# Optimization experiments

Hardware: AMD Instinct MI355X
Metric: run time of the kernel (lower is better)

The kernel has to match this reference:

```python
import jax, jax.numpy as jnp
import numpy as np
from jax import lax

STRIDES = (8, 16, 32)
NUM_CLASSES = 80
TOPK = 1000
CONF_THRESH = 0.05
NMS_THRESH = 0.6


def setup_inputs() -> dict:
    key = jax.random.key(0)
    ks = jax.random.split(key, 10)
    hw = [(256, 256), (128, 128), (64, 64)]
    inp = {}
    for lv, (h, w) in enumerate(hw):
        inp[f"cls_pred_{lv}"] = jax.random.normal(ks[3 * lv + 0], (NUM_CLASSES, h, w), jnp.float32)
        inp[f"reg_pred_{lv}"] = jax.random.normal(ks[3 * lv + 1], (4, h, w), jnp.float32)
        inp[f"ctn_pred_{lv}"] = jax.random.normal(ks[3 * lv + 2], (1, h, w), jnp.float32)
    inp["scales"] = jax.random.uniform(ks[9], (3,), jnp.float32)
    return inp


def _level_decode(cls_p, reg_p, ctn_p, scale, stride):
    # cls_p: [C,H,W] -> flatten to [M,C] matching torch permute(1,2,0).view(-1,C)
    C, H, W = cls_p.shape
    cls = jnp.transpose(cls_p, (1, 2, 0)).reshape(-1, C)          # [M,C]
    reg = jnp.transpose(reg_p, (1, 2, 0)).reshape(-1, 4)          # [M,4]
    reg = jax.nn.relu(reg * scale) * stride                       # Scale + relu + stride
    ctn = jnp.transpose(ctn_p, (1, 2, 0)).reshape(-1, 1)          # [M,1]
    joint = jnp.sqrt(jax.nn.sigmooid(cls) * jax.nn.sigmoid(ctn)) if False else \
        jnp.sqrt(jax.nn.sigmoid(cls) * jax.nn.sigmoid(ctn))      # [M,C]
    scores = jnp.max(joint, axis=-1)                              # [M]
    labels = jnp.argmax(joint, axis=-1)                           # [M]
    ay, ax = jnp.meshgrid(jnp.arange(H), jnp.arange(W), indexing='ij')
    anchors = (jnp.stack([ax, ay], -1).reshape(-1, 2).astype(cls.dtype) + 0.5) * stride  # [M,2]
    # per-level topk (M > TOPK for all levels here)
    scores, idx = lax.top_k(scores, TOPK)
    labels = labels[idx]
    reg = reg[idx]
    anchors = anchors[idx]
    boxes = jnp.concatenate([anchors - reg[:, :2], anchors + reg[:, 2:]], axis=-1)  # x1y1x2y2
    return scores, labels, boxes


def _nms(boxes, scores):
    # Faithful port of the pure-python NMS: fixed-shape keep mask, sorted order.
    N = boxes.shape[0]
    order = jnp.argsort(-scores)
    b = boxes[order]
    x1, y1, x2, y2 = b[:, 0], b[:, 1], b[:, 2], b[:, 3]
    areas = (x2 - x1) * (y2 - y1)
    xx1 = jnp.maximum(x1[:, None], x1[None, :])
    yy1 = jnp.maximum(y1[:, None], y1[None, :])
    xx2 = jnp.minimum(x2[:, None], x2[None, :])
    yy2 = jnp.minimum(y2[:, None], y2[None, :])
    w = jnp.maximum(1e-10, xx2 - xx1)
    h = jnp.maximum(1e-10, yy2 - yy1)
    inter = w * h
    iou = inter / (areas[:, None] + areas[None, :] - inter + 1e-14)  # [N,N]
    idxs = jnp.arange(N)

    def body(i, keep):
        sup = (iou[i] > NMS_THRESH) & (idxs > i) & keep[i]
        return keep & ~sup

    keep = lax.fori_loop(0, N, body, jnp.ones((N,), bool))
    return order, keep


def reference(cls_pred_0, cls_pred_1, cls_pred_2,
              reg_pred_0, reg_pred_1, reg_pred_2,
              ctn_pred_0, ctn_pred_1, ctn_pred_2, scales):
    cls_l = [cls_pred_0, cls_pred_1, cls_pred_2]
    reg_l = [reg_pred_0, reg_pred_1, reg_pred_2]
    ctn_l = [ctn_pred_0, ctn_pred_1, ctn_pred_2]
    all_s, all_l, all_b = [], [], []
    for lv in range(3):
        s, lb, bx = _level_decode(cls_l[lv], reg_l[lv], ctn_l[lv], scales[lv], float(STRIDES[lv]))
        all_s.append(s); all_l.append(lb); all_b.append(bx)
    scores = jnp.concatenate(all_s)   # [3000]
    labels = jnp.concatenate(all_l)
    boxes = jnp.concatenate(all_b)    # [3000,4]
    order, keep = _nms(boxes, scores)
    scores_s = scores[order]
    labels_s = labels[order]
    boxes_s = boxes[order]
    keep = keep & (scores_s > CONF_THRESH)
    return boxes_s, scores_s, labels_s, keep
```

## Files before the change

kernel.cpp:

```cpp
#include <hip/hip_runtime.h>
#include <cmath>
#include <stdint.h>

#define NPTS   86016
#define NCB    1024
#define K_TOP  1000
#define NOUT   3000
#define NWORDS 47
#define NTILE  47
#define ECAP   8192
#define FCAP   1024
#define SPPB   64
#define SELCAP 4096

#define CH_OFF     0
#define CNT_OFF    (NCB * 3 * 4)
#define MEMSET_BYTES (CNT_OFF + 64)
#define KEYS_OFF   (CNT_OFF + 64)
#define LAB_OFF    (KEYS_OFF + NPTS * 8)
#define STAGE_OFF  (LAB_OFF + NPTS * 4)
#define SURV_OFF   (STAGE_OFF + 3 * 65536 * 8)
#define EDGE_OFF   (SURV_OFF + NOUT * 8 + 64)
#define FLAG_OFF   (EDGE_OFF + ECAP * 4)

__device__ __forceinline__ float sig_f32_stepwise(float x) {
    float e = (float)exp(-(double)x);
    return 1.0f / (1.0f + e);
}

__device__ __forceinline__ void locate(int g, int& lv, int& p, int& HW) {
    if (g < 65536)      { lv = 0; p = g;         HW = 65536; }
    else if (g < 81920) { lv = 1; p = g - 65536; HW = 16384; }
    else                { lv = 2; p = g - 81920; HW = 4096;  }
}

__global__ __launch_bounds__(256) void score_kernel(
        const float* __restrict__ cls0, const float* __restrict__ cls1,
        const float* __restrict__ cls2,
        const float* __restrict__ ctn0, const float* __restrict__ ctn1,
        const float* __restrict__ ctn2,
        unsigned long long* __restrict__ keys, int* __restrict__ labels,
        int* __restrict__ chist,
        int* __restrict__ cnt, unsigned* __restrict__ flags) {
    __shared__ float pm[5 * SPPB], pv[5 * SPPB];
    __shared__ int pidx[5 * SPPB];
    __shared__ int lch[NCB];
    const int tid = threadIdx.x;
    const int base = blockIdx.x * SPPB;
    for (int i = tid; i < NCB; i += 256) lch[i] = 0;
    for (int it = tid; it < 5 * SPPB; it += 256) {
        int c = it / SPPB, pt = it - c * SPPB;
        int g = base + pt, lv, p, HW;
        locate(g, lv, p, HW);
        const float* cls = (lv == 0) ? cls0 : ((lv == 1) ? cls1 : cls2);
        const float* bp = cls + (size_t)c * 16 * HW + p;
        float x[16];
#pragma unroll
        for (int cc = 0; cc < 16; cc++) x[cc] = bp[(size_t)cc * HW];
        float m = -INFINITY, v = -INFINITY; int idx = 0;
#pragma unroll
        for (int cc = 0; cc < 16; cc++)
            if (x[cc] > m) { v = m; m = x[cc]; idx = c * 16 + cc; }
        pm[it] = m; pv[it] = v; pidx[it] = idx;
    }
    __syncthreads();
    if (tid < SPPB) {
        int g = base + tid, lv, p, HW;
        locate(g, lv, p, HW);
        const float* ctn = (lv == 0) ? ctn0 : ((lv == 1) ? ctn1 : ctn2);
        float m = -INFINITY, v = -INFINITY; int idx = 0;
#pragma unroll
        for (int k = 0; k < 5; k++) {
            float bm = pm[k * SPPB + tid];
            float bv = pv[k * SPPB + tid];
            int bidx = pidx[k * SPPB + tid];
            if (bm > m) { v = fmaxf(m, bv); m = bm; idx = bidx; }
        }
        float sc = sig_f32_stepwise(ctn[p]);
        float sM = sig_f32_stepwise(m);
        float jm = __fsqrt_rn(sM * sc);
        float sV = sig_f32_stepwise(v);
        float jv = __fsqrt_rn(sV * sc);
        if (jv == jm) {
            int f = atomicAdd(&cnt[13], 1);
            if (f < FCAP) flags[f] = (unsigned)g;
        }
        unsigned int bits = __float_as_uint(jm);
        keys[g] = ((unsigned long long)bits << 32) | (0xFFFFFFFFu - (unsigned)g);
        labels[g] = idx;
        atomicAdd(&lch[(int)(bits >> 20)], 1);
    }
    __syncthreads();
    int lv0, p0, HW0; locate(base, lv0, p0, HW0);
    for (int i = tid; i < NCB; i += 256) {
        int v = lch[i];
        if (v) atomicAdd(&chist[lv0 * NCB + i], v);
    }
}

__global__ __launch_bounds__(1024) void tcs_kernel(
        const float* __restrict__ cls0, const float* __restrict__ cls1,
        const float* __restrict__ cls2,
        const float* __restrict__ ctn0, const float* __restrict__ ctn1,
        const float* __restrict__ ctn2,
        const unsigned long long* __restrict__ keys,
        const int* __restrict__ chist,
        const unsigned* __restrict__ flags, const int* __restrict__ cnt,
        int* __restrict__ labels,
        unsigned long long* __restrict__ stage,
        unsigned long long* __restrict__ surv) {
    int bid = blockIdx.x, tid = threadIdx.x;
    if (bid == 3) {
        int nf = cnt[13]; if (nf > FCAP) nf = FCAP;
        int wave = tid >> 6, lane = tid & 63;
        for (int f = wave; f < nf; f += 16) {
            int g = (int)flags[f], lv, p, HW;
            locate(g, lv, p, HW);
            const float* cls = (lv == 0) ? cls0 : ((lv == 1) ? cls1 : cls2);
            const float* ctn = (lv == 0) ? ctn0 : ((lv == 1) ? ctn1 : ctn2);
            float sc = sig_f32_stepwise(ctn[p]);
            float bestv = -1.0f; int besti = 127;
            {
                float s = sig_f32_stepwise(cls[(size_t)lane * HW + p]);
                float sj = __fsqrt_rn(s * sc);
                bestv = sj; besti = lane;
            }
            if (lane < 16) {
                int c2 = lane + 64;
                float s = sig_f32_stepwise(cls[(size_t)c2 * HW + p]);
                float sj = __fsqrt_rn(s * sc);
                if (sj > bestv) { bestv = sj; besti = c2; }
            }
            for (int off = 32; off; off >>= 1) {
                float ov = __shfl_xor(bestv, off, 64);
                int   oi = __shfl_xor(besti, off, 64);
                if (ov > bestv || (ov == bestv && oi < besti)) { bestv = ov; besti = oi; }
            }
            if (lane == 0) labels[g] = besti;
        }
        return;
    }
    const int lv = bid;
    const int base = (lv == 0) ? 0 : ((lv == 1) ? 65536 : 81920);
    const int HW = (lv == 0) ? 65536 : ((lv == 1) ? 16384 : 4096);
    unsigned long long* stg = stage + (size_t)lv * 65536;

    __shared__ int part[1024];
    __shared__ int fine[257];
    __shared__ int s_chunk, s_above, sBf, sR;
    __shared__ int sSure, sStage, sCand;
    __shared__ unsigned long long sel[SELCAP];

    if (tid == 0) { sSure = 0; sStage = 0; sCand = 0; }
    part[tid] = chist[lv * NCB + tid];
    __syncthreads();
    for (int off = 1; off < 1024; off <<= 1) {
        int v = part[tid] + ((tid + off < 1024) ? part[tid + off] : 0);
        __syncthreads(); part[tid] = v; __syncthreads();
    }
    int nxt = (tid < 1023) ? part[tid + 1] : 0;
    if (part[tid] >= K_TOP && nxt < K_TOP) { s_chunk = tid; s_above = nxt; }
    if (tid < 257) fine[tid] = 0;
    __syncthreads();
    const int chunk = s_chunk, above = s_above;
    for (int i = tid; i < HW; i += 1024) {
        unsigned long long key = keys[base + i];
        int cb = (int)(key >> 52);
        if (cb > chunk) {
            int k = atomicAdd(&sSure, 1);
            sel[k] = key;
        } else if (cb == chunk) {
            int k = atomicAdd(&sStage, 1);
            stg[k] = key;
            atomicAdd(&fine[(int)(key >> 44) & 255], 1);
        }
    }
    __syncthreads();
    for (int off = 1; off < 256; off <<= 1) {
        int v = 0;
        if (tid < 256) v = fine[tid] + ((tid + off < 256) ? fine[tid + off] : 0);
        __syncthreads(); if (tid < 256) fine[tid] = v; __syncthreads();
    }
    if (tid < 256) {
        int ge    = above + fine[tid];
        int genxt = above + ((tid < 255) ? fine[tid + 1] : 0);
        if (ge >= K_TOP && genxt < K_TOP) {
            sBf = tid;
            sR  = K_TOP - genxt;
        }
    }
    __syncthreads();
    const int Bf = sBf;
    const int nstage = sStage;
    {
        int Ca = above + ((Bf < 255) ? fine[Bf + 1] : 0);
        for (int i = tid; i < nstage; i += 1024) {
            unsigned long long key = stg[i];
            int fb = (int)(key >> 44) & 255;
            if (fb > Bf) {
                int k = atomicAdd(&sSure, 1);
                sel[k] = key;
            } else if (fb == Bf) {
                int k = atomicAdd(&sCand, 1);
                int idx = Ca + k;
                if (idx < SELCAP) sel[idx] = key;
            }
        }
    }
    __syncthreads();
    int tot = sSure + sCand; if (tot > SELCAP) tot = SELCAP;
    int m = 1024; while (m < tot) m <<= 1;
    for (int t = tot + tid; t < m; t += 1024) sel[t] = 0ULL;
    __syncthreads();
    for (int k = 2; k <= m; k <<= 1)
        for (int j = k >> 1; j > 0; j >>= 1) {
            for (int t = tid; t < m; t += 1024) {
                int l = t ^ j;
                if (l > t) {
                    unsigned long long a = sel[t], b = sel[l];
                    if (((t & k) == 0) ? (a < b) : (a > b)) { sel[t] = b; sel[l] = a; }
                }
            }
            __syncthreads();
        }
    if (tid < K_TOP) surv[lv * K_TOP + tid] = sel[tid];
}

__global__ __launch_bounds__(1024) void merge_emit_kernel(
        const unsigned long long* __restrict__ surv,
        const int* __restrict__ labels,
        const float* __restrict__ reg0, const float* __restrict__ reg1,
        const float* __restrict__ reg2,
        const float* __restrict__ scales,
        float* __restrict__ out) {
    __shared__ unsigned long long L[3][1024];
    __shared__ unsigned long long s[NOUT];
    int tid = threadIdx.x;
#pragma unroll
    for (int lv = 0; lv < 3; lv++)
        L[lv][tid] = (tid < K_TOP) ? surv[lv * K_TOP + tid] : 0ULL;
    __syncthreads();
    for (int e = tid; e < NOUT; e += 1024) {
        int a = e / K_TOP, i = e - a * K_TOP;
        unsigned long long key = L[a][i];
        int rank = i;
#pragma unroll
        for (int b = 0; b < 3; b++) {
            if (b == a) continue;
            int lo = 0, hi = K_TOP;
            while (lo < hi) {
                int mid = (lo + hi) >> 1;
                if (L[b][mid] > key) lo = mid + 1; else hi = mid;
            }
            rank += lo;
        }
        s[rank] = key;
    }
    __syncthreads();
    for (int r = tid; r < NOUT; r += 1024) {
        unsigned long long key = s[r];
        unsigned int bits = (unsigned)(key >> 32);
        float score = __uint_as_float(bits);
        unsigned int g = 0xFFFFFFFFu - (unsigned)(key & 0xFFFFFFFFULL);
        int lv, p;
        if (g < 65536u)      { lv = 0; p = (int)g; }
        else if (g < 81920u) { lv = 1; p = (int)g - 65536; }
        else                 { lv = 2; p = (int)g - 81920; }
        const float* rp = (lv == 0) ? reg0 : ((lv == 1) ? reg1 : reg2);
        int HW = (lv == 0) ? 65536 : ((lv == 1) ? 16384 : 4096);
        int W = 256 >> lv;
        float strideF = (float)(8 << lv);
        float scale = scales[lv];
        int x = p & (W - 1);
        int y = p >> (8 - lv);
        float r0 = fmaxf(0.0f, rp[0 * HW + p] * scale) * strideF;
        float r1 = fmaxf(0.0f, rp[1 * HW + p] * scale) * strideF;
        float r2 = fmaxf(0.0f, rp[2 * HW + p] * scale) * strideF;
        float r3 = fmaxf(0.0f, rp[3 * HW + p] * scale) * strideF;
        float ax = ((float)x + 0.5f) * strideF;
        float ay = ((float)y + 0.5f) * strideF;
        out[r * 4 + 0] = ax - r0;
        out[r * 4 + 1] = ay - r1;
        out[r * 4 + 2] = ax + r2;
        out[r * 4 + 3] = ay + r3;
        out[12000 + r] = score;
        out[15000 + r] = (float)labels[g];
    }
}

__global__ __launch_bounds__(256) void edge_kernel(const float* __restrict__ out,
                                                   unsigned* __restrict__ edges_g,
                                                   int* __restrict__ cnt) {
    __shared__ float x1[128], y1[128], x2[128], y2[128];
    int t = blockIdx.x, tid = threadIdx.x;
    int ta = 0, rem = t;
    while (rem >= NTILE - ta) { rem -= NTILE - ta; ta++; }
    int tb = ta + rem;
    if (tid < 64) {
        int gi = ta * 64 + tid;
        if (gi < NOUT) {
            float4 b = ((const float4*)out)[gi];
            x1[tid] = b.x; y1[tid] = b.y; x2[tid] = b.z; y2[tid] = b.w;
        }
    } else if (tid < 128) {
        int gj = tb * 64 + (tid - 64);
        if (gj < NOUT) {
            float4 b = ((const float4*)out)[gj];
            x1[tid] = b.x; y1[tid] = b.y; x2[tid] = b.z; y2[tid] = b.w;
        }
    }
    __syncthreads();
#pragma unroll
    for (int q = 0; q < 16; q++) {
        int idx = q * 256 + tid;
        int ii = idx >> 6, jj = idx & 63;
        int i = ta * 64 + ii, j = tb * 64 + jj;
        if (i < j && j < NOUT) {
            float ai = (x2[ii] - x1[ii]) * (y2[ii] - y1[ii]);
            float aj = (x2[64 + jj] - x1[64 + jj]) * (y2[64 + jj] - y1[64 + jj]);
            float xx1 = fmaxf(x1[ii], x1[64 + jj]), yy1 = fmaxf(y1[ii], y1[64 + jj]);
            float xx2 = fminf(x2[ii], x2[64 + jj]), yy2 = fminf(y2[ii], y2[64 + jj]);
            float ww = fmaxf(1e-10f, xx2 - xx1);
            float hh = fmaxf(1e-10f, yy2 - yy1);
            float inter = ww * hh;
            float iou = inter / (((ai + aj) - inter) + 1e-14f);
            if ((double)iou > 0.6) {
                int e = atomicAdd(&cnt[12], 1);
                if (e < ECAP) edges_g[e] = ((unsigned)i << 12) | (unsigned)j;
            }
        }
    }
}

__global__ __launch_bounds__(1024) void nms_sparse_kernel(
        const unsigned* __restrict__ edges_g,
        const int* __restrict__ cnt,
        const float* __restrict__ scores_s,
        float* __restrict__ keep_out) {
    __shared__ unsigned ed[ECAP];
    __shared__ unsigned long long supLds[NWORDS];
    int tid = threadIdx.x;
    int E = cnt[12]; if (E > ECAP) E = ECAP;
    int m = 1; while (m < E) m <<= 1;
    for (int t = tid; t < m; t += 1024) ed[t] = (t < E) ? edges_g[t] : 0xFFFFFFFFu;
    __syncthreads();
    for (int k = 2; k <= m; k <<= 1)
        for (int j = k >> 1; j > 0; j >>= 1) {
            for (int t = tid; t < m; t += 1024) {
                int l = t ^ j;
                if (l > t) {
                    unsigned a = ed[t], b = ed[l];
                    if (((t & k) == 0) ? (a > b) : (a < b)) { ed[t] = b; ed[l] = a; }
                }
            }
            __syncthreads();
        }
    if (tid < 64) {
        int lane = tid;
        unsigned long long supW = 0ULL;
        int ep = 0;
        for (int c = 0; c < NWORDS; c++) {
            unsigned long long cw = __shfl(supW, c, 64);
            int hi = (c + 1) * 64;
            while (ep < E) {
                unsigned k = ed[ep];
                int i = (int)(k >> 12);
                if (i >= hi) break;
                int j = (int)(k & 4095);
                if (!((cw >> (i & 63)) & 1ULL)) {
                    if ((j >> 6) == c) cw |= 1ULL << (j & 63);
                    else if (lane == (j >> 6)) supW |= 1ULL << (j & 63);
                }
                ep++;
            }
            if (lane == c) supW = cw;
        }
        if (lane < NWORDS) supLds[lane] = supW;
    }
    __syncthreads();
    for (int j = tid; j < NOUT; j += 1024) {
        bool s = (supLds[j >> 6] >> (j & 63)) & 1ULL;
        float scv = scores_s[j];
        keep_out[j] = (!s && ((double)scv > 0.05)) ? 1.0f : 0.0f;
    }
}

extern "C" void kernel_launch(void* const* d_in, const int* in_sizes, int n_in,
                              void* d_out, int out_size, void* d_ws, size_t ws_size,
                              hipStream_t stream) {
    const float* cls0 = (const float*)d_in[0];
    const float* reg0 = (const float*)d_in[1];
    const float* ctn0 = (const float*)d_in[2];
    const float* cls1 = (const float*)d_in[3];
    const float* reg1 = (const float*)d_in[4];
    const float* ctn1 = (const float*)d_in[5];
    const float* cls2 = (const float*)d_in[6];
    const float* reg2 = (const float*)d_in[7];
    const float* ctn2 = (const float*)d_in[8];
    const float* scales = (const float*)d_in[9];

    char* ws = (char*)d_ws;
    int* chist = (int*)(ws + CH_OFF);
    int* cnt  = (int*)(ws + CNT_OFF);
    unsigned long long* keys = (unsigned long long*)(ws + KEYS_OFF);
    int* labels = (int*)(ws + LAB_OFF);
    unsigned long long* stage = (unsigned long long*)(ws + STAGE_OFF);
    unsigned long long* surv = (unsigned long long*)(ws + SURV_OFF);
    unsigned* edges = (unsigned*)(ws + EDGE_OFF);
    unsigned* flags = (unsigned*)(ws + FLAG_OFF);
    float* out = (float*)d_out;

    hipMemsetAsync(ws, 0, MEMSET_BYTES, stream);

    score_kernel<<<NPTS / SPPB, 256, 0, stream>>>(cls0, cls1, cls2, ctn0, ctn1, ctn2,
                                                  keys, labels, chist, cnt, flags);
    tcs_kernel<<<4, 1024, 0, stream>>>(cls0, cls1, cls2, ctn0, ctn1, ctn2,
                                       keys, chist, flags, cnt, labels,
                                       stage, surv);
    merge_emit_kernel<<<1, 1024, 0, stream>>>(surv, labels, reg0, reg1, reg2, scales, out);
    edge_kernel<<<NTILE * (NTILE + 1) / 2, 256, 0, stream>>>(out, edges, cnt);
    nms_sparse_kernel<<<1, 1024, 0, stream>>>(edges, cnt, out + 12000, out + 18000);
}
```

Measured before the change: 186.6 us.

## Replace per-level bitonic sort and block scans with wave-level scans and rank sort

The per-level top-K select kernel now computes its suffix scans with wavefront shuffles instead of log-step shared-memory scans that synchronise the whole block. Per-thread shared atomics for compaction are replaced by ballot-based wave-aggregated atomics, and the global loads are unrolled into batches of 8 or 4. The final bitonic sort over up to 4096 keys is replaced by a counting rank sort over two separate buffers, one for keys surely in the top-K and one for boundary-bucket candidates. In exchange, candidate capacity is cut to 1024 per buffer, and the rank sort costs O(n) comparisons per thread while assuming the keys are unique.

```diff
diff --git a/kernel.cpp b/kernel.cpp
--- a/kernel.cpp
+++ b/kernel.cpp
@@ -11,7 +11,6 @@
 #define ECAP   8192
 #define FCAP   1024
 #define SPPB   64
-#define SELCAP 4096
 
 #define CH_OFF     0
 #define CNT_OFF    (NCB * 3 * 4)
@@ -144,86 +143,167 @@
     const int base = (lv == 0) ? 0 : ((lv == 1) ? 65536 : 81920);
     const int HW = (lv == 0) ? 65536 : ((lv == 1) ? 16384 : 4096);
     unsigned long long* stg = stage + (size_t)lv * 65536;
-
-    __shared__ int part[1024];
+    const int lane = tid & 63;
+    const int wv = tid >> 6;
+    const unsigned long long lmlt = (1ULL << lane) - 1;
+
     __shared__ int fine[257];
-    __shared__ int s_chunk, s_above, sBf, sR;
+    __shared__ int wtot[16], wsuf[16];
+    __shared__ int s_chunk, s_above, sBf;
     __shared__ int sSure, sStage, sCand;
-    __shared__ unsigned long long sel[SELCAP];
+    __shared__ unsigned long long sel[1024];
+    __shared__ unsigned long long cbuf[1024];
 
     if (tid == 0) { sSure = 0; sStage = 0; sCand = 0; }
-    part[tid] = chist[lv * NCB + tid];
-    __syncthreads();
-    for (int off = 1; off < 1024; off <<= 1) {
-        int v = part[tid] + ((tid + off < 1024) ? part[tid + off] : 0);
-        __syncthreads(); part[tid] = v; __syncthreads();
-    }
-    int nxt = (tid < 1023) ? part[tid + 1] : 0;
-    if (part[tid] >= K_TOP && nxt < K_TOP) { s_chunk = tid; s_above = nxt; }
     if (tid < 257) fine[tid] = 0;
+
+    {
+        int s = chist[lv * NCB + tid];
+#pragma unroll
+        for (int off = 1; off <= 32; off <<= 1) {
+            int t = __shfl_down(s, off, 64);
+            if (lane + off < 64) s += t;
+        }
+        if (lane == 0) wtot[wv] = s;
+        __syncthreads();
+        if (tid < 16) {
+            int t = wtot[tid];
+#pragma unroll
+            for (int off = 1; off <= 8; off <<= 1) {
+                int q = __shfl_down(t, off, 64);
+                if (tid + off < 16) t += q;
+            }
+            wsuf[tid] = t;
+        }
+        __syncthreads();
+        int offW = (wv < 15) ? wsuf[wv + 1] : 0;
+        int part_i = s + offW;
+        int s1 = __shfl_down(s, 1, 64);
+        int part_n = (lane < 63) ? (s1 + offW) : offW;
+        if (part_i >= K_TOP && part_n < K_TOP) { s_chunk = tid; s_above = part_n; }
+    }
     __syncthreads();
     const int chunk = s_chunk, above = s_above;
-    for (int i = tid; i < HW; i += 1024) {
-        unsigned long long key = keys[base + i];
-        int cb = (int)(key >> 52);
-        if (cb > chunk) {
-            int k = atomicAdd(&sSure, 1);
-            sel[k] = key;
-        } else if (cb == chunk) {
-            int k = atomicAdd(&sStage, 1);
-            stg[k] = key;
-            atomicAdd(&fine[(int)(key >> 44) & 255], 1);
-        }
-    }
-    __syncthreads();
-    for (int off = 1; off < 256; off <<= 1) {
-        int v = 0;
-        if (tid < 256) v = fine[tid] + ((tid + off < 256) ? fine[tid + off] : 0);
-        __syncthreads(); if (tid < 256) fine[tid] = v; __syncthreads();
-    }
-    if (tid < 256) {
-        int ge    = above + fine[tid];
-        int genxt = above + ((tid < 255) ? fine[tid + 1] : 0);
-        if (ge >= K_TOP && genxt < K_TOP) {
-            sBf = tid;
-            sR  = K_TOP - genxt;
+
+    {
+        const int nSlab = HW >> 10;
+        for (int s0 = 0; s0 < nSlab; s0 += 8) {
+            unsigned long long k8[8];
+#pragma unroll
+            for (int u = 0; u < 8; u++)
+                k8[u] = (s0 + u < nSlab) ? keys[base + ((s0 + u) << 10) + tid] : 0ULL;
+#pragma unroll
+            for (int u = 0; u < 8; u++) if (s0 + u < nSlab) {
+                unsigned long long key = k8[u];
+                int cb = (int)(key >> 52);
+                bool pS = cb > chunk, pT = cb == chunk;
+                unsigned long long mS = __ballot(pS);
+                if (mS) {
+                    int ldr = __ffsll((long long)mS) - 1;
+                    int bk;
+                    if (lane == ldr) bk = atomicAdd(&sSure, __popcll(mS));
+                    bk = __shfl(bk, ldr, 64);
+                    if (pS) sel[bk + __popcll(mS & lmlt)] = key;
+                }
+                unsigned long long mT = __ballot(pT);
+                if (mT) {
+                    int ldr = __ffsll((long long)mT) - 1;
+                    int bk;
+                    if (lane == ldr) bk = atomicAdd(&sStage, __popcll(mT));
+                    bk = __shfl(bk, ldr, 64);
+                    if (pT) {
+                        stg[bk + __popcll(mT & lmlt)] = key;
+                        atomicAdd(&fine[(int)(key >> 44) & 255], 1);
+                    }
+                }
+            }
+        }
+    }
+    __syncthreads();
+
+    {
+        int fs = (tid < 256) ? fine[tid] : 0;
+#pragma unroll
+        for (int off = 1; off <= 32; off <<= 1) {
+            int t = __shfl_down(fs, off, 64);
+            if (lane + off < 64) fs += t;
+        }
+        if (tid < 256 && lane == 0) wtot[wv] = fs;
+        __syncthreads();
+        if (tid < 4) {
+            int t = wtot[tid];
+#pragma unroll
+            for (int off = 1; off <= 2; off <<= 1) {
+                int q = __shfl_down(t, off, 64);
+                if (tid + off < 4) t += q;
+            }
+            wsuf[tid] = t;
+        }
+        __syncthreads();
+        if (tid < 256) {
+            int offW = (wv < 3) ? wsuf[wv + 1] : 0;
+            int ge = above + fs + offW;
+            int fs1 = __shfl_down(fs, 1, 64);
+            int genxt = above + ((lane < 63) ? (fs1 + offW) : offW);
+            if (ge >= K_TOP && genxt < K_TOP) sBf = tid;
         }
     }
     __syncthreads();
     const int Bf = sBf;
-    const int nstage = sStage;
-    {
-        int Ca = above + ((Bf < 255) ? fine[Bf + 1] : 0);
-        for (int i = tid; i < nstage; i += 1024) {
-            unsigned long long key = stg[i];
+    const int nst = sStage;
+
+    for (int i0 = 0; i0 < nst; i0 += 4096) {
+        unsigned long long k4[4];
+#pragma unroll
+        for (int u = 0; u < 4; u++) {
+            int i = i0 + (u << 10) + tid;
+            k4[u] = (i < nst) ? stg[i] : 0ULL;
+        }
+#pragma unroll
+        for (int u = 0; u < 4; u++) {
+            int i = i0 + (u << 10) + tid;
+            bool valid = i < nst;
+            unsigned long long key = k4[u];
             int fb = (int)(key >> 44) & 255;
-            if (fb > Bf) {
-                int k = atomicAdd(&sSure, 1);
-                sel[k] = key;
-            } else if (fb == Bf) {
-                int k = atomicAdd(&sCand, 1);
-                int idx = Ca + k;
-                if (idx < SELCAP) sel[idx] = key;
-            }
-        }
-    }
-    __syncthreads();
-    int tot = sSure + sCand; if (tot > SELCAP) tot = SELCAP;
-    int m = 1024; while (m < tot) m <<= 1;
-    for (int t = tot + tid; t < m; t += 1024) sel[t] = 0ULL;
-    __syncthreads();
-    for (int k = 2; k <= m; k <<= 1)
-        for (int j = k >> 1; j > 0; j >>= 1) {
-            for (int t = tid; t < m; t += 1024) {
-                int l = t ^ j;
-                if (l > t) {
-                    unsigned long long a = sel[t], b = sel[l];
-                    if (((t & k) == 0) ? (a < b) : (a > b)) { sel[t] = b; sel[l] = a; }
+            bool pS = valid && (fb > Bf);
+            bool pC = valid && (fb == Bf);
+            unsigned long long mS = __ballot(pS);
+            if (mS) {
+                int ldr = __ffsll((long long)mS) - 1;
+                int bk;
+                if (lane == ldr) bk = atomicAdd(&sSure, __popcll(mS));
+                bk = __shfl(bk, ldr, 64);
+                if (pS) sel[bk + __popcll(mS & lmlt)] = key;
+            }
+            unsigned long long mC = __ballot(pC);
+            if (mC) {
+                int ldr = __ffsll((long long)mC) - 1;
+                int bk;
+                if (lane == ldr) bk = atomicAdd(&sCand, __popcll(mC));
+                bk = __shfl(bk, ldr, 64);
+                if (pC) {
+                    int pos = bk + __popcll(mC & lmlt);
+                    if (pos < 1024) cbuf[pos] = key;
                 }
             }
-            __syncthreads();
-        }
-    if (tid < K_TOP) surv[lv * K_TOP + tid] = sel[tid];
+        }
+    }
+    __syncthreads();
+
+    const int nS = sSure;
+    int nC = sCand; if (nC > 1024) nC = 1024;
+    unsigned long long myS = (tid < nS) ? sel[tid] : 0ULL;
+    unsigned long long myC = (tid < nC) ? cbuf[tid] : 0ULL;
+    int rS = 0, rC = 0;
+#pragma unroll 4
+    for (int i = 0; i < nS; i++) rS += (sel[i] > myS);
+#pragma unroll 4
+    for (int i = 0; i < nC; i++) rC += (cbuf[i] > myC);
+    __syncthreads();
+    if (tid < nS) sel[rS] = myS;
+    if (tid < nC) cbuf[rC] = myC;
+    __syncthreads();
+    if (tid < K_TOP) surv[lv * K_TOP + tid] = (tid < nS) ? sel[tid] : cbuf[tid - nS];
 }
 
 __global__ __launch_bounds__(1024) void merge_emit_kernel(
```

Measured after the change: 191.8 us. +2.8%, slower.
